# Performance work log

Measured on AMD Instinct MI355X. Metric: run time of the kernel, lower is better.

Reference implementation:

```python
import jax, jax.numpy as jnp
import numpy as np
from jax import lax

N_POINTS = 4_194_304
HIDDEN = 16
N_HIDDEN_LAYERS = 8   # num_layers=9 -> 1 input layer + 8 bias-free hidden layers


def setup_inputs() -> dict:
    key = jax.random.key(0)
    k_x, k_win, k_bin, k_wh, k_wout = jax.random.split(key, 5)
    x = jax.random.uniform(k_x, (N_POINTS, 2), dtype=jnp.float32)
    # PyTorch Linear default init: U(-1/sqrt(fan_in), 1/sqrt(fan_in))
    s_in = 1.0 / np.sqrt(2.0)
    s_h = 1.0 / np.sqrt(HIDDEN)
    W_in = jax.random.uniform(k_win, (HIDDEN, 2), jnp.float32, -s_in, s_in)
    b_in = jax.random.uniform(k_bin, (HIDDEN,), jnp.float32, -s_in, s_in)
    W_hidden = jax.random.uniform(k_wh, (N_HIDDEN_LAYERS, HIDDEN, HIDDEN), jnp.float32, -s_h, s_h)
    W_out = jax.random.uniform(k_wout, (3, HIDDEN), jnp.float32, -s_h, s_h)
    return {"x": x, "W_in": W_in, "b_in": b_in, "W_hidden": W_hidden, "W_out": W_out}


def reference(x, W_in, b_in, W_hidden, W_out):
    # [N,2] -> [N,16], biased input layer + tanh
    h = jnp.tanh(x @ W_in.T + b_in)
    # 8 bias-free 16x16 layers, each followed by tanh
    def step(h, W):
        return jnp.tanh(h @ W.T), None
    h, _ = lax.scan(step, h, W_hidden)
    # output layer 16 -> 3, sigmoid to map to [0,1] RGB
    return jax.nn.sigmoid(h @ W_out.T)
```

## Files before the change

### kernel.cpp

```cpp
#include <hip/hip_runtime.h>


typedef float  f32x4 __attribute__((ext_vector_type(4)));
typedef __fp16 f16x4 __attribute__((ext_vector_type(4)));
typedef __fp16 f16x2 __attribute__((ext_vector_type(2)));

#define K2   2.8853900817779268f
#define KOUT (-1.4426950408889634f)

__device__ __forceinline__ f16x4 v4s(f32x4 y) {
    float e0 = __builtin_amdgcn_exp2f(y[0]);
    float e1 = __builtin_amdgcn_exp2f(y[1]);
    float e2 = __builtin_amdgcn_exp2f(y[2]);
    float e3 = __builtin_amdgcn_exp2f(y[3]);
    float d0 = e0 + 1.0f, d1 = e1 + 1.0f, d2 = e2 + 1.0f, d3 = e3 + 1.0f;
    float p01 = d0 * d1, p23 = d2 * d3;
    float r   = __builtin_amdgcn_rcpf(p01 * p23);
    float i01 = r * p23, i23 = r * p01;
    float v0 = i01 * d1, v1 = i01 * d0;
    float v2 = i23 * d3, v3 = i23 * d2;
    f16x2 lo = __builtin_amdgcn_cvt_pkrtz(v0, v1);
    f16x2 hi = __builtin_amdgcn_cvt_pkrtz(v2, v3);
    return __builtin_shufflevector(lo, hi, 0, 1, 2, 3);
}

__global__ __launch_bounds__(256, 6)
void artnet_kernel(const float2* __restrict__ x,
                   const float2* __restrict__ Win,
                   const float*  __restrict__ bin,
                   const float4* __restrict__ Wh,
                   const float4* __restrict__ Wout,
                   float* __restrict__ out,
                   int nPairs, int nWaves)
{
    const int tid  = blockIdx.x * 256 + threadIdx.x;
    const int gw   = tid >> 6;
    const int lane = threadIdx.x & 63;
    const int row  = lane & 15;
    const int quad = lane >> 4;

    f16x4 aw[8];
    f32x4 crs[8];
#pragma unroll
    for (int l = 0; l < 8; ++l) {
        float4 w = Wh[l * 64 + row * 4 + quad];
        const float s = -2.0f * K2;
        f16x2 lo = __builtin_amdgcn_cvt_pkrtz(w.x * s, w.y * s);
        f16x2 hi = __builtin_amdgcn_cvt_pkrtz(w.z * s, w.w * s);
        aw[l] = __builtin_shufflevector(lo, hi, 0, 1, 2, 3);
        float partial = w.x + w.y + w.z + w.w;
        partial += __shfl_xor(partial, 16, 64);
        partial += __shfl_xor(partial, 32, 64);
        f32x4 c;
#pragma unroll
        for (int i = 0; i < 4; ++i)
            c[i] = K2 * __shfl(partial, quad * 4 + i, 64);
        crs[l] = c;
    }

    f16x4 awin = {(__fp16)0.0f, (__fp16)0.0f, (__fp16)0.0f, (__fp16)0.0f};
    if (quad == 0) {
        float2 wr = Win[row];
        f16x2 lo = __builtin_amdgcn_cvt_pkrtz(wr.x * K2, wr.y * K2);
        f16x2 hi = __builtin_amdgcn_cvt_pkrtz(bin[row] * K2, 0.0f);
        awin = __builtin_shufflevector(lo, hi, 0, 1, 2, 3);
    }

    f16x4 awo = {(__fp16)0.0f, (__fp16)0.0f, (__fp16)0.0f, (__fp16)0.0f};
    float prt = 0.0f;
    if (row < 3) {
        float4 w = Wout[row * 4 + quad];
        const float s = -2.0f * KOUT;
        f16x2 lo = __builtin_amdgcn_cvt_pkrtz(w.x * s, w.y * s);
        f16x2 hi = __builtin_amdgcn_cvt_pkrtz(w.z * s, w.w * s);
        awo = __builtin_shufflevector(lo, hi, 0, 1, 2, 3);
        prt = w.x + w.y + w.z + w.w;
    }
    prt += __shfl_xor(prt, 16, 64);
    prt += __shfl_xor(prt, 32, 64);
    f32x4 crso;
#pragma unroll
    for (int i = 0; i < 4; ++i)
        crso[i] = KOUT * __shfl(prt, quad * 4 + i, 64);

    const f32x4 zero4 = {0.0f, 0.0f, 0.0f, 0.0f};
    const f16x2 one0  = {(__fp16)1.0f, (__fp16)0.0f};

    for (int pi = gw; pi < nPairs; pi += nWaves) {
        const int t0 = pi * 2;
        f16x4 bf[2];
        f32x4 acco[2];

#pragma unroll
        for (int s = 0; s < 2; ++s) {
            float2 xv = x[(t0 + s) * 16 + row];
            f16x2 lo = __builtin_amdgcn_cvt_pkrtz(xv.x, xv.y);
            bf[s] = __builtin_shufflevector(lo, one0, 0, 1, 2, 3);
        }
#pragma unroll
        for (int s = 0; s < 2; ++s) {
            f32x4 acc = __builtin_amdgcn_mfma_f32_16x16x16f16(awin, bf[s], zero4, 0, 0, 0);
            bf[s] = v4s(acc);
        }

#pragma unroll
        for (int l = 0; l < 8; ++l) {
#pragma unroll
            for (int s = 0; s < 2; ++s) {
                f32x4 acc = __builtin_amdgcn_mfma_f32_16x16x16f16(aw[l], bf[s], crs[l], 0, 0, 0);
                bf[s] = v4s(acc);
            }
        }

#pragma unroll
        for (int s = 0; s < 2; ++s)
            acco[s] = __builtin_amdgcn_mfma_f32_16x16x16f16(awo, bf[s], crso, 0, 0, 0);

        if (quad == 0) {
            float ea0 = __builtin_amdgcn_exp2f(acco[0][0]);
            float ea1 = __builtin_amdgcn_exp2f(acco[0][1]);
            float ea2 = __builtin_amdgcn_exp2f(acco[0][2]);
            float eb0 = __builtin_amdgcn_exp2f(acco[1][0]);
            float eb1 = __builtin_amdgcn_exp2f(acco[1][1]);
            float eb2 = __builtin_amdgcn_exp2f(acco[1][2]);
            float da0 = ea0 + 1.0f, da1 = ea1 + 1.0f, da2 = ea2 + 1.0f;
            float db0 = eb0 + 1.0f, db1 = eb1 + 1.0f, db2 = eb2 + 1.0f;
            float pa01 = da0 * da1, P3a = pa01 * da2;
            float pb01 = db0 * db1, P3b = pb01 * db2;
            float r  = __builtin_amdgcn_rcpf(P3a * P3b);
            float rA = r * P3b, rB = r * P3a;
            float sa2 = rA * pa01;
            float ia  = rA * da2;
            float sa0 = ia * da1, sa1 = ia * da0;
            float sb2 = rB * pb01;
            float ib  = rB * db2;
            float sb0 = ib * db1, sb1 = ib * db0;
            const int p0 = t0 * 16 + row;
            out[p0 * 3 + 0] = sa0;
            out[p0 * 3 + 1] = sa1;
            out[p0 * 3 + 2] = sa2;
            const int p1 = p0 + 16;
            out[p1 * 3 + 0] = sb0;
            out[p1 * 3 + 1] = sb1;
            out[p1 * 3 + 2] = sb2;
        }
    }
}

extern "C" void kernel_launch(void* const* d_in, const int* in_sizes, int n_in,
                              void* d_out, int out_size, void* d_ws, size_t ws_size,
                              hipStream_t stream) {
    const float2* x    = (const float2*)d_in[0];
    const float2* Win  = (const float2*)d_in[1];
    const float*  bin  = (const float*) d_in[2];
    const float4* Wh   = (const float4*)d_in[3];
    const float4* Wout = (const float4*)d_in[4];
    float* out = (float*)d_out;

    const int n      = in_sizes[0] / 2;
    const int nPairs = n / 32;
    const int blocks = 4096;
    const int nWaves = blocks * 4;

    artnet_kernel<<<blocks, 256, 0, stream>>>(x, Win, bin, Wh, Wout, out, nPairs, nWaves);
}
```

Baseline: 195.3 us.

## Move per-layer bias constants to LDS and prefetch next input pair

The eight per-layer f32x4 bias-correction vectors no longer sit in registers. They are written to shared memory once per block and read back inside the layer loop, with the next layer's vector loaded one step ahead. This is meant to cut VGPR pressure, which is 32 registers per lane. The loop also becomes software-pipelined, loading the next iteration's x values before the current MLP runs so global-load latency overlaps compute. In exchange, each iteration now does extra LDS reads and there is a block-level barrier.

```diff
diff --git a/kernel.cpp b/kernel.cpp
--- a/kernel.cpp
+++ b/kernel.cpp
@@ -39,8 +39,9 @@
     const int row  = lane & 15;
     const int quad = lane >> 4;
 
+    __shared__ __align__(16) float crs_lds[8][16];
+
     f16x4 aw[8];
-    f32x4 crs[8];
 #pragma unroll
     for (int l = 0; l < 8; ++l) {
         float4 w = Wh[l * 64 + row * 4 + quad];
@@ -51,11 +52,8 @@
         float partial = w.x + w.y + w.z + w.w;
         partial += __shfl_xor(partial, 16, 64);
         partial += __shfl_xor(partial, 32, 64);
-        f32x4 c;
-#pragma unroll
-        for (int i = 0; i < 4; ++i)
-            c[i] = K2 * __shfl(partial, quad * 4 + i, 64);
-        crs[l] = c;
+        if (threadIdx.x < 16)
+            crs_lds[l][row] = K2 * partial;
     }
 
     f16x4 awin = {(__fp16)0.0f, (__fp16)0.0f, (__fp16)0.0f, (__fp16)0.0f};
@@ -83,46 +81,59 @@
     for (int i = 0; i < 4; ++i)
         crso[i] = KOUT * __shfl(prt, quad * 4 + i, 64);
 
+    __syncthreads();
+
     const f32x4 zero4 = {0.0f, 0.0f, 0.0f, 0.0f};
     const f16x2 one0  = {(__fp16)1.0f, (__fp16)0.0f};
 
-    for (int pi = gw; pi < nPairs; pi += nWaves) {
+    int pi = gw;
+    float2 xa, xb;
+    if (pi < nPairs) {
+        xa = x[pi * 32 + row];
+        xb = x[pi * 32 + 16 + row];
+    }
+
+    while (pi < nPairs) {
+        const int pn = pi + nWaves;
         const int t0 = pi * 2;
-        f16x4 bf[2];
-        f32x4 acco[2];
 
-#pragma unroll
-        for (int s = 0; s < 2; ++s) {
-            float2 xv = x[(t0 + s) * 16 + row];
-            f16x2 lo = __builtin_amdgcn_cvt_pkrtz(xv.x, xv.y);
-            bf[s] = __builtin_shufflevector(lo, one0, 0, 1, 2, 3);
-        }
-#pragma unroll
-        for (int s = 0; s < 2; ++s) {
-            f32x4 acc = __builtin_amdgcn_mfma_f32_16x16x16f16(awin, bf[s], zero4, 0, 0, 0);
-            bf[s] = v4s(acc);
+        f16x2 la = __builtin_amdgcn_cvt_pkrtz(xa.x, xa.y);
+        f16x2 lb = __builtin_amdgcn_cvt_pkrtz(xb.x, xb.y);
+        f16x4 bf0 = __builtin_shufflevector(la, one0, 0, 1, 2, 3);
+        f16x4 bf1 = __builtin_shufflevector(lb, one0, 0, 1, 2, 3);
+
+        if (pn < nPairs) {
+            xa = x[pn * 32 + row];
+            xb = x[pn * 32 + 16 + row];
         }
 
+        f32x4 a0 = __builtin_amdgcn_mfma_f32_16x16x16f16(awin, bf0, zero4, 0, 0, 0);
+        f32x4 a1 = __builtin_amdgcn_mfma_f32_16x16x16f16(awin, bf1, zero4, 0, 0, 0);
+        bf0 = v4s(a0);
+        bf1 = v4s(a1);
+
+        f32x4 crsN = *(const f32x4*)&crs_lds[0][quad * 4];
 #pragma unroll
         for (int l = 0; l < 8; ++l) {
-#pragma unroll
-            for (int s = 0; s < 2; ++s) {
-                f32x4 acc = __builtin_amdgcn_mfma_f32_16x16x16f16(aw[l], bf[s], crs[l], 0, 0, 0);
-                bf[s] = v4s(acc);
-            }
+            f32x4 crsC = crsN;
+            if (l < 7)
+                crsN = *(const f32x4*)&crs_lds[l + 1][quad * 4];
+            f32x4 y0 = __builtin_amdgcn_mfma_f32_16x16x16f16(aw[l], bf0, crsC, 0, 0, 0);
+            f32x4 y1 = __builtin_amdgcn_mfma_f32_16x16x16f16(aw[l], bf1, crsC, 0, 0, 0);
+            bf0 = v4s(y0);
+            bf1 = v4s(y1);
         }
 
-#pragma unroll
-        for (int s = 0; s < 2; ++s)
-            acco[s] = __builtin_amdgcn_mfma_f32_16x16x16f16(awo, bf[s], crso, 0, 0, 0);
+        f32x4 acco0 = __builtin_amdgcn_mfma_f32_16x16x16f16(awo, bf0, crso, 0, 0, 0);
+        f32x4 acco1 = __builtin_amdgcn_mfma_f32_16x16x16f16(awo, bf1, crso, 0, 0, 0);
 
         if (quad == 0) {
-            float ea0 = __builtin_amdgcn_exp2f(acco[0][0]);
-            float ea1 = __builtin_amdgcn_exp2f(acco[0][1]);
-            float ea2 = __builtin_amdgcn_exp2f(acco[0][2]);
-            float eb0 = __builtin_amdgcn_exp2f(acco[1][0]);
-            float eb1 = __builtin_amdgcn_exp2f(acco[1][1]);
-            float eb2 = __builtin_amdgcn_exp2f(acco[1][2]);
+            float ea0 = __builtin_amdgcn_exp2f(acco0[0]);
+            float ea1 = __builtin_amdgcn_exp2f(acco0[1]);
+            float ea2 = __builtin_amdgcn_exp2f(acco0[2]);
+            float eb0 = __builtin_amdgcn_exp2f(acco1[0]);
+            float eb1 = __builtin_amdgcn_exp2f(acco1[1]);
+            float eb2 = __builtin_amdgcn_exp2f(acco1[2]);
             float da0 = ea0 + 1.0f, da1 = ea1 + 1.0f, da2 = ea2 + 1.0f;
             float db0 = eb0 + 1.0f, db1 = eb1 + 1.0f, db2 = eb2 + 1.0f;
             float pa01 = da0 * da1, P3a = pa01 * da2;
@@ -144,6 +155,8 @@
             out[p1 * 3 + 1] = sb1;
             out[p1 * 3 + 2] = sb2;
         }
+
+        pi = pn;
     }
 }
 
```

Result: faster. 187.6 us (-4.0%).
